# Kernel optimization log

Measured on AMD Instinct MI355X. Metric: run time of the kernel, lower is better.

Reference implementation:

```python
import jax, jax.numpy as jnp
import numpy as np

BATCH, SEQ, DIM, NH = 2, 4096, 1024, 16
HD = DIM // NH
BLOCK = 64


def setup_inputs() -> dict:
    key = jax.random.key(0)
    ks = jax.random.split(key, 8)
    x = jax.random.normal(ks[0], (BATCH, SEQ, DIM), dtype=jnp.float32)
    # standard RoPE tables: (seq, head_dim)
    inv_freq = 1.0 / (10000.0 ** (jnp.arange(0, HD, 2, dtype=jnp.float32) / HD))
    t = jnp.arange(SEQ, dtype=jnp.float32)
    freqs = jnp.outer(t, inv_freq)                      # (SEQ, HD//2)
    emb = jnp.concatenate([freqs, freqs], axis=-1)      # (SEQ, HD)
    cos, sin = jnp.cos(emb), jnp.sin(emb)
    s = 0.02
    wq = jax.random.normal(ks[1], (DIM, DIM), jnp.float32) * s
    wk = jax.random.normal(ks[2], (DIM, DIM), jnp.float32) * s
    wv = jax.random.normal(ks[3], (DIM, DIM), jnp.float32) * s
    wo = jax.random.normal(ks[4], (DIM, DIM), jnp.float32) * s
    A_log = jax.random.normal(ks[5], (NH,), jnp.float32) * 0.1
    w_dt_w = jax.random.normal(ks[6], (DIM, NH), jnp.float32) * s
    w_dt_b = jnp.zeros((NH,), jnp.float32)
    return {"x": x, "cos": cos, "sin": sin, "wq": wq, "wk": wk, "wv": wv,
            "wo": wo, "A_log": A_log, "w_dt_w": w_dt_w, "w_dt_b": w_dt_b}


def segsum(a):
    """a: (..., T) -> (..., T, T) lower-triangular segment sums, -inf above diag."""
    T = a.shape[-1]
    cs = jnp.cumsum(a, axis=-1)
    seg = cs[..., :, None] - cs[..., None, :]
    mask = jnp.tril(jnp.ones((T, T), dtype=bool))
    return jnp.where(mask, seg, -jnp.inf)


def rotate_half(t):
    t1, t2 = jnp.split(t, 2, axis=-1)
    return jnp.concatenate([-t2, t1], axis=-1)


def ssd(X, A, B, C, block_len):
    """Mamba-2 SSD chunked scan.
    X: (b,l,h,p)  A: (b,l,h)  B,C: (b,l,h,n)
    """
    b, l, h, p = X.shape
    c = l // block_len
    Xc = X.reshape(b, c, block_len, h, p)
    Bc = B.reshape(b, c, block_len, h, -1)
    Cc = C.reshape(b, c, block_len, h, -1)
    Ac = jnp.transpose(A.reshape(b, c, block_len, h), (0, 3, 1, 2))  # (b,h,c,l)
    A_cumsum = jnp.cumsum(Ac, axis=-1)
    # intra-chunk (diagonal block) output
    L = jnp.exp(segsum(Ac))                                          # (b,h,c,l,l)
    Y_diag = jnp.einsum('bclhn,bcshn,bhcls,bcshp->bclhp', Cc, Bc, L, Xc)
    # per-chunk states
    decay_states = jnp.exp(A_cumsum[:, :, :, -1:] - A_cumsum)        # (b,h,c,l)
    states = jnp.einsum('bclhn,bhcl,bclhp->bchpn', Bc, decay_states, Xc)
    init = jnp.zeros_like(states[:, :1])
    states = jnp.concatenate([init, states], axis=1)                 # (b,c+1,h,p,n)
    # inter-chunk recurrence (done as a 1-SS matmul over chunk axis)
    A_last = jnp.pad(A_cumsum[:, :, :, -1], ((0, 0), (0, 0), (1, 0)))
    decay_chunk = jnp.exp(segsum(A_last))                            # (b,h,c+1,c+1)
    new_states = jnp.einsum('bhzc,bchpn->bzhpn', decay_chunk, states)
    states, final_state = new_states[:, :-1], new_states[:, -1]
    # state -> output contribution
    state_decay_out = jnp.exp(A_cumsum)
    Y_off = jnp.einsum('bclhn,bchpn,bhcl->bclhp', Cc, states, state_decay_out)
    Y = (Y_diag + Y_off).reshape(b, l, h, p)
    return Y, final_state


def reference(x, cos, sin, wq, wk, wv, wo, A_log, w_dt_w, w_dt_b):
    b, l, dim = x.shape
    h = A_log.shape[0]
    d = dim // h
    xq = (x @ wq).reshape(b, l, h, d)
    xk = (x @ wk).reshape(b, l, h, d)
    xv = (x @ wv).reshape(b, l, h, d)
    cb = cos[None, :, None, :]
    sb = sin[None, :, None, :]
    xq = xq * cb + rotate_half(xq) * sb
    xk = xk * cb + rotate_half(xk) * sb
    dt = jax.nn.softplus(x @ w_dt_w + w_dt_b)           # (b,l,h)
    A = -jnp.exp(A_log)[None, None, :] * dt             # (b,l,h)
    X = xv * dt[..., None]                              # (b,l,h,d)
    Y, state = ssd(X, A, xk, xq, BLOCK)
    # replicate torch's transpose(1,2).view(b, l, -1) exactly:
    y = jnp.transpose(Y, (0, 2, 1, 3)).reshape(b, l, h * d)
    return y @ wo, state
```

## Files before the change

kernel.cpp:

```cpp
#include <hip/hip_runtime.h>


typedef __bf16 bf16x8 __attribute__((ext_vector_type(8)));
typedef float f32x4 __attribute__((ext_vector_type(4)));
typedef unsigned int u32x4 __attribute__((ext_vector_type(4)));
typedef unsigned short u16x8 __attribute__((ext_vector_type(8)));
typedef unsigned short u16x4 __attribute__((ext_vector_type(4)));

__device__ __forceinline__ unsigned short f2bf(float f) {
  unsigned int u = __builtin_bit_cast(unsigned int, f);
  u += 0x7fffu + ((u >> 16) & 1u);
  return (unsigned short)(u >> 16);
}
__device__ __forceinline__ float bf2f(unsigned short s) {
  unsigned int u = ((unsigned int)s) << 16;
  return __builtin_bit_cast(float, u);
}

#define GLOAD16(gp, lp)                                                \
  __builtin_amdgcn_global_load_lds(                                    \
      (const __attribute__((address_space(1))) void*)(gp),             \
      (__attribute__((address_space(3))) void*)(lp), 16, 0, 0)

__global__ __launch_bounds__(256) void convert_bf16_kernel(
    const float* __restrict__ in, unsigned short* __restrict__ out, int n4,
    const float* __restrict__ wdt, unsigned short* __restrict__ wdt_bf) {
  const int bx = blockIdx.x;
  if (bx < 8192) {
    int g = bx * 256 + threadIdx.x;
    if (g < n4) {
      f32x4 v = *reinterpret_cast<const f32x4*>(in + (size_t)g * 4);
      u16x4 o;
      o.x = f2bf(v.x); o.y = f2bf(v.y); o.z = f2bf(v.z); o.w = f2bf(v.w);
      *reinterpret_cast<u16x4*>(out + (size_t)g * 4) = o;
    }
  } else {
    const int g = (bx - 8192) * 256 + threadIdx.x;
    const int n = g >> 10, k = g & 1023;
    wdt_bf[g] = f2bf(wdt[k * 16 + n]);
  }
}

__global__ __launch_bounds__(256) void transpose_w_kernel(
    const float* __restrict__ w0, const float* __restrict__ w1,
    const float* __restrict__ w2, const float* __restrict__ w3,
    unsigned short* __restrict__ wt) {
  __shared__ float tile[32][33];
  const int z = blockIdx.z;
  const float* w = (z == 0) ? w0 : (z == 1) ? w1 : (z == 2) ? w2 : w3;
  unsigned short* o = wt + (size_t)z * 1024 * 1024;
  const int bx = blockIdx.x, by = blockIdx.y;
  const int tx = threadIdx.x, ty = threadIdx.y;
#pragma unroll
  for (int i = 0; i < 4; ++i)
    tile[ty + i * 8][tx] = w[(size_t)(by * 32 + ty + i * 8) * 1024 + bx * 32 + tx];
  __syncthreads();
#pragma unroll
  for (int i = 0; i < 4; ++i)
    o[(size_t)(bx * 32 + ty + i * 8) * 1024 + by * 32 + tx] = f2bf(tile[tx][ty + i * 8]);
}

__global__ __launch_bounds__(256) void dt_gemm_kernel(
    const unsigned short* __restrict__ A,
    const unsigned short* __restrict__ Bt,
    const float* __restrict__ bdt, float* __restrict__ dt) {
  __shared__ unsigned short As[2 * 64 * 32];
  const int tid = threadIdx.x, lane = tid & 63, w = tid >> 6;
  const int m0 = blockIdx.x * 64;
  const unsigned short* ga =
      A + (size_t)(m0 + w * 16 + (lane >> 2)) * 1024 + (lane & 3) * 8;
  unsigned short* la = As + w * 512;
  const int lr = lane & 15, lk = (lane >> 4) * 8;
  const unsigned short* gb = Bt + (size_t)lr * 1024 + lk;
  f32x4 acc = {};
  for (int kt = 0; kt < 1024; kt += 64) {
    GLOAD16(ga + kt, la);
    GLOAD16(ga + kt + 32, la + 2048);
    bf16x8 bF0 = *reinterpret_cast<const bf16x8*>(gb + kt);
    bf16x8 bF1 = *reinterpret_cast<const bf16x8*>(gb + kt + 32);
    __syncthreads();
    bf16x8 aF0 = *reinterpret_cast<const bf16x8*>(&As[(w * 16 + lr) * 32 + lk]);
    bf16x8 aF1 = *reinterpret_cast<const bf16x8*>(&As[2048 + (w * 16 + lr) * 32 + lk]);
    acc = __builtin_amdgcn_mfma_f32_16x16x32_bf16(aF0, bF0, acc, 0, 0, 0);
    acc = __builtin_amdgcn_mfma_f32_16x16x32_bf16(aF1, bF1, acc, 0, 0, 0);
    __syncthreads();
  }
  const int h = lr;
  const float bv = bdt[h];
#pragma unroll
  for (int r = 0; r < 4; ++r) {
    const int row = m0 + w * 16 + (lane >> 4) * 4 + r;
    const float a = acc[r] + bv;
    const float sp = (a > 0.f) ? (a + log1pf(expf(-a))) : log1pf(expf(a));
    dt[(size_t)row * 16 + h] = sp;
  }
}

template <int EPI>
__global__ __launch_bounds__(256) void gemm128_kernel(
    const unsigned short* __restrict__ A, const unsigned short* __restrict__ Bt,
    void* __restrict__ out0, unsigned short* __restrict__ out1,
    unsigned short* __restrict__ out2, const float* __restrict__ cosb,
    const float* __restrict__ sinb, const float* __restrict__ dtb) {
  __shared__ unsigned short As[128 * 64];
  __shared__ unsigned short Bs[128 * 64];
  const int tid = threadIdx.x, lane = tid & 63, w = tid >> 6;
  const int m0 = blockIdx.y * 128, n0 = blockIdx.x * 128;
  const int rw = lane >> 3;
  const int cu = ((lane & 7) ^ rw) * 8;
  const unsigned short* ga = A + (size_t)(m0 + w * 8 + rw) * 1024 + cu;
  const unsigned short* gb = Bt + (size_t)(n0 + w * 8 + rw) * 1024 + cu;
  unsigned short* la = As + (w * 8) * 64;
  unsigned short* lb = Bs + (w * 8) * 64;
  const int lr = lane & 15, lku = lane >> 4;
  const int wr = w >> 1, wc = w & 1;
  const int xr = lr & 7;
  f32x4 acc[4][4] = {};
  for (int kt = 0; kt < 1024; kt += 64) {
#pragma unroll
    for (int g = 0; g < 4; ++g) {
      GLOAD16(ga + kt + (size_t)(g * 32) * 1024, la + g * 32 * 64);
      GLOAD16(gb + kt + (size_t)(g * 32) * 1024, lb + g * 32 * 64);
    }
    __syncthreads();
#pragma unroll
    for (int kk = 0; kk < 2; ++kk) {
      const int un = (kk * 4 + lku) ^ xr;
      bf16x8 aF[4], bF[4];
#pragma unroll
      for (int i = 0; i < 4; ++i) {
        aF[i] = *reinterpret_cast<const bf16x8*>(&As[(wr * 64 + i * 16 + lr) * 64 + un * 8]);
        bF[i] = *reinterpret_cast<const bf16x8*>(&Bs[(wc * 64 + i * 16 + lr) * 64 + un * 8]);
      }
#pragma unroll
      for (int i = 0; i < 4; ++i)
#pragma unroll
        for (int j = 0; j < 4; ++j)
          acc[i][j] = __builtin_amdgcn_mfma_f32_16x16x32_bf16(aF[i], bF[j], acc[i][j], 0, 0, 0);
    }
    __syncthreads();
  }
  const int r0 = m0 + wr * 64 + ((lane >> 4) << 2);
  if constexpr (EPI == 0) {
    float* O = (float*)out0;
    const int c0 = n0 + wc * 64 + lr;
#pragma unroll
    for (int i = 0; i < 4; ++i)
#pragma unroll
      for (int j = 0; j < 4; ++j)
#pragma unroll
        for (int r = 0; r < 4; ++r)
          O[(size_t)(r0 + i * 16 + r) * 1024 + c0 + j * 16] = acc[i][j][r];
  } else {
    const int col = n0 + wc * 64;
    if (col < 2048) {
      unsigned short* O = (col < 1024) ? (unsigned short*)out0 : out1;
      const int cbase = col & 1023;
#pragma unroll
      for (int i = 0; i < 4; ++i)
#pragma unroll
        for (int jj = 0; jj < 2; ++jj) {
          const int d1 = jj * 16 + lr;
#pragma unroll
          for (int r = 0; r < 4; ++r) {
            const int row = r0 + i * 16 + r;
            const int l = row & 4095;
            const float cv = cosb[(size_t)l * 64 + d1];
            const float sv = sinb[(size_t)l * 64 + d1];
            const float v1 = acc[i][jj][r], v2 = acc[i][jj + 2][r];
            O[(size_t)row * 1024 + cbase + jj * 16 + lr] = f2bf(v1 * cv - v2 * sv);
            O[(size_t)row * 1024 + cbase + jj * 16 + lr + 32] = f2bf(v2 * cv + v1 * sv);
          }
        }
    } else {
      unsigned short* O = out2;
      const int cbase = col - 2048;
      const int h = cbase >> 6;
#pragma unroll
      for (int i = 0; i < 4; ++i)
#pragma unroll
        for (int r = 0; r < 4; ++r) {
          const int row = r0 + i * 16 + r;
          const float dtv = dtb[(size_t)row * 16 + h];
#pragma unroll
          for (int j = 0; j < 4; ++j)
            O[(size_t)row * 1024 + cbase + j * 16 + lr] = f2bf(acc[i][j][r] * dtv);
        }
    }
  }
}

__global__ __launch_bounds__(256) void ssd_states_kernel(
    const unsigned short* __restrict__ Kb, const unsigned short* __restrict__ Xb,
    const float* __restrict__ dtb, const float* __restrict__ A_log,
    unsigned short* __restrict__ chunk_states, float* __restrict__ chunk_dec) {
  __shared__ unsigned short T1[64 * 72], T2[64 * 72];
  __shared__ unsigned short BtL[64 * 72], XdL[64 * 72];
  __shared__ float csL[64], decL[64];
  const int c = blockIdx.x, h = blockIdx.y, b = blockIdx.z;
  const int tid = threadIdx.x, lane = tid & 63, w = tid >> 6;
  const size_t gbase = ((size_t)(b * 4096 + c * 64)) * 1024 + h * 64;
  {
    const int s = tid >> 2, e0 = (tid & 3) * 16;
    const unsigned short* gk = Kb + gbase + (size_t)s * 1024 + e0;
    const unsigned short* gx = Xb + gbase + (size_t)s * 1024 + e0;
    *(u32x4*)&T1[s * 72 + e0] = *(const u32x4*)gk;
    *(u32x4*)&T1[s * 72 + e0 + 8] = *(const u32x4*)(gk + 8);
    *(u32x4*)&T2[s * 72 + e0] = *(const u32x4*)gx;
    *(u32x4*)&T2[s * 72 + e0 + 8] = *(const u32x4*)(gx + 8);
  }
  if (w == 0) {
    float a = -expf(A_log[h]) * dtb[((size_t)(b * 4096 + c * 64 + lane)) * 16 + h];
    float v = a;
#pragma unroll
    for (int d = 1; d < 64; d <<= 1) {
      float o = __shfl_up(v, d, 64);
      if (lane >= d) v += o;
    }
    const float tot = __shfl(v, 63, 64);
    csL[lane] = v;
    decL[lane] = expf(tot - v);
    if (lane == 0) chunk_dec[((size_t)(b * 16 + h)) * 64 + c] = expf(tot);
  }
  __syncthreads();
#pragma unroll
  for (int q = 0; q < 2; ++q) {
    const int p = lane;
    const int s0 = (q * 4 + w) * 8;
    u16x8 vb, vx;
#pragma unroll
    for (int j = 0; j < 8; ++j) {
      vb[j] = T1[(s0 + j) * 72 + p];
      vx[j] = f2bf(bf2f(T2[(s0 + j) * 72 + p]) * decL[s0 + j]);
    }
    *(u16x8*)&BtL[p * 72 + s0] = vb;
    *(u16x8*)&XdL[p * 72 + s0] = vx;
  }
  __syncthreads();
  const int lr = lane & 15, lk = (lane >> 4) * 8;
  f32x4 acc[4] = {};
#pragma unroll
  for (int kt = 0; kt < 64; kt += 32) {
    bf16x8 aF = *reinterpret_cast<const bf16x8*>(&XdL[(w * 16 + lr) * 72 + kt + lk]);
#pragma unroll
    for (int j = 0; j < 4; ++j) {
      bf16x8 bF = *reinterpret_cast<const bf16x8*>(&BtL[(j * 16 + lr) * 72 + kt + lk]);
      acc[j] = __builtin_amdgcn_mfma_f32_16x16x32_bf16(aF, bF, acc[j], 0, 0, 0);
    }
  }
  const size_t stb = ((size_t)((b * 64 + c) * 16 + h)) * 4096;
#pragma unroll
  for (int j = 0; j < 4; ++j)
#pragma unroll
    for (int r = 0; r < 4; ++r)
      chunk_states[stb + (size_t)(w * 16 + (lane >> 4) * 4 + r) * 64 + j * 16 + lr] =
          f2bf(acc[j][r]);
}

__global__ __launch_bounds__(256) void scan_kernel(
    const unsigned short* __restrict__ chunk_states, const float* __restrict__ chunk_dec,
    unsigned short* __restrict__ inc_bf, float* __restrict__ state_out) {
  __shared__ float decs[64];
  const int g = blockIdx.x * 256 + threadIdx.x;
  const int n = g & 63, p = (g >> 6) & 63, h = (g >> 12) & 15, b = g >> 16;
  if (threadIdx.x < 64)
    decs[threadIdx.x] = chunk_dec[(size_t)((blockIdx.x * 256) >> 12 & 15) * 64 +
                                  (size_t)(blockIdx.x >> 8) * 1024 + threadIdx.x];
  __syncthreads();
  const size_t pn = (size_t)p * 64 + n;
  const size_t stride = (size_t)16 * 4096;
  const size_t base0 = ((size_t)(b * 64) * 16 + h) * 4096 + pn;
  float inc = 0.f;
  float cur = bf2f(chunk_states[base0]);
  for (int c = 0; c < 64; ++c) {
    const size_t idx = base0 + (size_t)c * stride;
    inc_bf[idx] = f2bf(inc);
    float nxt = (c < 63) ? bf2f(chunk_states[idx + stride]) : 0.f;
    inc = decs[c] * inc + cur;
    cur = nxt;
  }
  state_out[((size_t)(b * 16 + h) * 64 + p) * 64 + n] = inc;
}

__global__ __launch_bounds__(256) void ssd_y_kernel(
    const unsigned short* __restrict__ Qb, const unsigned short* __restrict__ Kb,
    const unsigned short* __restrict__ Xb, const unsigned short* __restrict__ Sg,
    const float* __restrict__ dtb, const float* __restrict__ A_log,
    unsigned short* __restrict__ y_bf) {
  __shared__ unsigned short Cb[64 * 72], Bb[64 * 72], Sb[64 * 72];
  __shared__ unsigned short Xt[64 * 72], TG[64 * 72];
  __shared__ float csL[64], sdeL[64];
  const int c = blockIdx.x, h = blockIdx.y, b = blockIdx.z;
  const int tid = threadIdx.x, lane = tid & 63, w = tid >> 6;
  const size_t gbase = ((size_t)(b * 4096 + c * 64)) * 1024 + h * 64;
  const size_t sbase = ((size_t)((b * 64 + c) * 16 + h)) * 4096;
  {
    const int s = tid >> 2, e0 = (tid & 3) * 16;
    const unsigned short* gq = Qb + gbase + (size_t)s * 1024 + e0;
    const unsigned short* gk = Kb + gbase + (size_t)s * 1024 + e0;
    const unsigned short* gx = Xb + gbase + (size_t)s * 1024 + e0;
    const unsigned short* gs = Sg + sbase + (size_t)s * 64 + e0;
    *(u32x4*)&Cb[s * 72 + e0] = *(const u32x4*)gq;
    *(u32x4*)&Cb[s * 72 + e0 + 8] = *(const u32x4*)(gq + 8);
    *(u32x4*)&Bb[s * 72 + e0] = *(const u32x4*)gk;
    *(u32x4*)&Bb[s * 72 + e0 + 8] = *(const u32x4*)(gk + 8);
    *(u32x4*)&TG[s * 72 + e0] = *(const u32x4*)gx;
    *(u32x4*)&TG[s * 72 + e0 + 8] = *(const u32x4*)(gx + 8);
    *(u32x4*)&Sb[s * 72 + e0] = *(const u32x4*)gs;
    *(u32x4*)&Sb[s * 72 + e0 + 8] = *(const u32x4*)(gs + 8);
  }
  if (w == 0) {
    float a = -expf(A_log[h]) * dtb[((size_t)(b * 4096 + c * 64 + lane)) * 16 + h];
    float v = a;
#pragma unroll
    for (int d = 1; d < 64; d <<= 1) {
      float o = __shfl_up(v, d, 64);
      if (lane >= d) v += o;
    }
    csL[lane] = v;
    sdeL[lane] = expf(v);
  }
  __syncthreads();
  const int lr = lane & 15, lk = (lane >> 4) * 8;
  f32x4 g[4] = {};
#pragma unroll
  for (int kt = 0; kt < 64; kt += 32) {
    bf16x8 aF = *reinterpret_cast<const bf16x8*>(&Cb[(w * 16 + lr) * 72 + kt + lk]);
#pragma unroll
    for (int j = 0; j < 4; ++j) {
      bf16x8 bF = *reinterpret_cast<const bf16x8*>(&Bb[(j * 16 + lr) * 72 + kt + lk]);
      g[j] = __builtin_amdgcn_mfma_f32_16x16x32_bf16(aF, bF, g[j], 0, 0, 0);
    }
  }
#pragma unroll
  for (int q = 0; q < 2; ++q) {
    const int p = lane;
    const int s0 = (q * 4 + w) * 8;
    u16x8 vx;
#pragma unroll
    for (int j = 0; j < 8; ++j) vx[j] = TG[(s0 + j) * 72 + p];
    *(u16x8*)&Xt[p * 72 + s0] = vx;
  }
  __syncthreads();
#pragma unroll
  for (int j = 0; j < 4; ++j)
#pragma unroll
    for (int r = 0; r < 4; ++r) {
      const int l = w * 16 + (lane >> 4) * 4 + r;
      const int s = j * 16 + lr;
      const float gm = (l >= s) ? g[j][r] * expf(csL[l] - csL[s]) : 0.f;
      TG[l * 72 + s] = f2bf(gm);
    }
  {
    const int rl = tid >> 2, e0 = (tid & 3) * 16;
    const float sde = sdeL[rl];
#pragma unroll
    for (int half = 0; half < 2; ++half) {
      u16x8 v = *(u16x8*)&Cb[rl * 72 + e0 + half * 8];
#pragma unroll
      for (int j = 0; j < 8; ++j) v[j] = f2bf(bf2f(v[j]) * sde);
      *(u16x8*)&Cb[rl * 72 + e0 + half * 8] = v;
    }
  }
  __syncthreads();
  f32x4 acc[4] = {};
#pragma unroll
  for (int kt = 0; kt < 64; kt += 32) {
    bf16x8 aG = *reinterpret_cast<const bf16x8*>(&TG[(w * 16 + lr) * 72 + kt + lk]);
    bf16x8 aC = *reinterpret_cast<const bf16x8*>(&Cb[(w * 16 + lr) * 72 + kt + lk]);
#pragma unroll
    for (int j = 0; j < 4; ++j) {
      bf16x8 bX = *reinterpret_cast<const bf16x8*>(&Xt[(j * 16 + lr) * 72 + kt + lk]);
      bf16x8 bS = *reinterpret_cast<const bf16x8*>(&Sb[(j * 16 + lr) * 72 + kt + lk]);
      acc[j] = __builtin_amdgcn_mfma_f32_16x16x32_bf16(aG, bX, acc[j], 0, 0, 0);
      acc[j] = __builtin_amdgcn_mfma_f32_16x16x32_bf16(aC, bS, acc[j], 0, 0, 0);
    }
  }
  const size_t orow = (size_t)b * 4096 + h * 256 + c * 4 + w;
#pragma unroll
  for (int j = 0; j < 4; ++j)
#pragma unroll
    for (int r = 0; r < 4; ++r) {
      const int li = (lane >> 4) * 4 + r;
      y_bf[orow * 1024 + li * 64 + j * 16 + lr] = f2bf(acc[j][r]);
    }
}

extern "C" void kernel_launch(void* const* d_in, const int* in_sizes, int n_in,
                              void* d_out, int out_size, void* d_ws, size_t ws_size,
                              hipStream_t stream) {
  (void)in_sizes; (void)n_in; (void)out_size; (void)ws_size;
  const float* x = (const float*)d_in[0];
  const float* cosb = (const float*)d_in[1];
  const float* sinb = (const float*)d_in[2];
  const float* wq = (const float*)d_in[3];
  const float* wk = (const float*)d_in[4];
  const float* wv = (const float*)d_in[5];
  const float* wo = (const float*)d_in[6];
  const float* A_log = (const float*)d_in[7];
  const float* wdt = (const float*)d_in[8];
  const float* bdt = (const float*)d_in[9];

  float* out_y = (float*)d_out;
  float* out_state = out_y + 8388608;

  const size_t MBB = 1048576;
  char* ws = (char*)d_ws;
  unsigned short* x_bf = (unsigned short*)(ws);
  unsigned short* w_t = (unsigned short*)(ws + 16 * MBB);
  unsigned short* q_bf = (unsigned short*)(ws + 24 * MBB);
  unsigned short* k_bf = (unsigned short*)(ws + 40 * MBB);
  unsigned short* xv_bf = (unsigned short*)(ws + 56 * MBB);
  float* dtb = (float*)(ws + 72 * MBB);
  unsigned short* wdt_bf = (unsigned short*)(ws + 73 * MBB);
  unsigned short* chunk_states = (unsigned short*)(ws + 74 * MBB);
  float* chunk_dec = (float*)(ws + 90 * MBB);
  unsigned short* inc_bf = (unsigned short*)(ws + 91 * MBB);

  convert_bf16_kernel<<<8256, 256, 0, stream>>>(x, x_bf, 2097152, wdt, wdt_bf);
  transpose_w_kernel<<<dim3(32, 32, 4), dim3(32, 8), 0, stream>>>(wq, wk, wv, wo, w_t);
  dt_gemm_kernel<<<128, 256, 0, stream>>>(x_bf, wdt_bf, bdt, dtb);

  gemm128_kernel<3><<<dim3(24, 64), 256, 0, stream>>>(
      x_bf, w_t, q_bf, k_bf, xv_bf, cosb, sinb, dtb);

  ssd_states_kernel<<<dim3(64, 16, 2), 256, 0, stream>>>(k_bf, xv_bf, dtb, A_log,
                                                         chunk_states, chunk_dec);
  scan_kernel<<<512, 256, 0, stream>>>(chunk_states, chunk_dec, inc_bf, out_state);
  ssd_y_kernel<<<dim3(64, 16, 2), 256, 0, stream>>>(q_bf, k_bf, xv_bf, inc_bf, dtb, A_log,
                                                    x_bf );

  gemm128_kernel<0><<<dim3(8, 64), 256, 0, stream>>>(
      x_bf , w_t + 3 * MBB, out_y, nullptr, nullptr, nullptr, nullptr, nullptr);
}
```

Before: 162.4 us.

## Merge conversion and weight-transpose kernels, deepen scan prefetch, tidy swizzle index

Combines the x/w_dt bf16 conversion and the four weight transposes into one prep kernel launch, so one launch and the gap between the two kernels go away. The scan kernel now prefetches chunk states two iterations ahead instead of one, to hide more load latency in its serial loop. The GEMM swizzle offset is precomputed in element units, which is cosmetic. The merged kernel uses a block-index branch with shared memory used only in the transpose path.

```diff
diff --git a/kernel.cpp b/kernel.cpp
--- a/kernel.cpp
+++ b/kernel.cpp
@@ -22,42 +22,40 @@
       (const __attribute__((address_space(1))) void*)(gp),             \
       (__attribute__((address_space(3))) void*)(lp), 16, 0, 0)
 
-__global__ __launch_bounds__(256) void convert_bf16_kernel(
-    const float* __restrict__ in, unsigned short* __restrict__ out, int n4,
-    const float* __restrict__ wdt, unsigned short* __restrict__ wdt_bf) {
-  const int bx = blockIdx.x;
-  if (bx < 8192) {
-    int g = bx * 256 + threadIdx.x;
-    if (g < n4) {
-      f32x4 v = *reinterpret_cast<const f32x4*>(in + (size_t)g * 4);
-      u16x4 o;
-      o.x = f2bf(v.x); o.y = f2bf(v.y); o.z = f2bf(v.z); o.w = f2bf(v.w);
-      *reinterpret_cast<u16x4*>(out + (size_t)g * 4) = o;
-    }
-  } else {
-    const int g = (bx - 8192) * 256 + threadIdx.x;
-    const int n = g >> 10, k = g & 1023;
-    wdt_bf[g] = f2bf(wdt[k * 16 + n]);
-  }
-}
-
-__global__ __launch_bounds__(256) void transpose_w_kernel(
+__global__ __launch_bounds__(256) void prep_kernel(
+    const float* __restrict__ x, unsigned short* __restrict__ x_bf,
+    const float* __restrict__ wdt, unsigned short* __restrict__ wdt_bf,
     const float* __restrict__ w0, const float* __restrict__ w1,
     const float* __restrict__ w2, const float* __restrict__ w3,
     unsigned short* __restrict__ wt) {
-  __shared__ float tile[32][33];
-  const int z = blockIdx.z;
-  const float* w = (z == 0) ? w0 : (z == 1) ? w1 : (z == 2) ? w2 : w3;
-  unsigned short* o = wt + (size_t)z * 1024 * 1024;
-  const int bx = blockIdx.x, by = blockIdx.y;
-  const int tx = threadIdx.x, ty = threadIdx.y;
-#pragma unroll
-  for (int i = 0; i < 4; ++i)
-    tile[ty + i * 8][tx] = w[(size_t)(by * 32 + ty + i * 8) * 1024 + bx * 32 + tx];
-  __syncthreads();
-#pragma unroll
-  for (int i = 0; i < 4; ++i)
-    o[(size_t)(bx * 32 + ty + i * 8) * 1024 + by * 32 + tx] = f2bf(tile[tx][ty + i * 8]);
+  const int bx = blockIdx.x;
+  const int tid = threadIdx.x;
+  if (bx < 8192) {
+    const int g = bx * 256 + tid;
+    f32x4 v = *reinterpret_cast<const f32x4*>(x + (size_t)g * 4);
+    u16x4 o;
+    o.x = f2bf(v.x); o.y = f2bf(v.y); o.z = f2bf(v.z); o.w = f2bf(v.w);
+    *reinterpret_cast<u16x4*>(x_bf + (size_t)g * 4) = o;
+  } else if (bx < 8256) {
+    const int g = (bx - 8192) * 256 + tid;
+    const int n = g >> 10, k = g & 1023;
+    wdt_bf[g] = f2bf(wdt[k * 16 + n]);
+  } else {
+    __shared__ float tile[32][33];
+    const int t = bx - 8256;
+    const int z = t >> 10, by = (t >> 5) & 31, bxx = t & 31;
+    const float* w = (z == 0) ? w0 : (z == 1) ? w1 : (z == 2) ? w2 : w3;
+    unsigned short* o = wt + (size_t)z * 1024 * 1024;
+    const int tx = tid & 31, ty = tid >> 5;
+#pragma unroll
+    for (int i = 0; i < 4; ++i)
+      tile[ty + i * 8][tx] = w[(size_t)(by * 32 + ty + i * 8) * 1024 + bxx * 32 + tx];
+    __syncthreads();
+#pragma unroll
+    for (int i = 0; i < 4; ++i)
+      o[(size_t)(bxx * 32 + ty + i * 8) * 1024 + by * 32 + tx] =
+          f2bf(tile[tx][ty + i * 8]);
+  }
 }
 
 __global__ __launch_bounds__(256) void dt_gemm_kernel(
@@ -125,12 +123,12 @@
     __syncthreads();
 #pragma unroll
     for (int kk = 0; kk < 2; ++kk) {
-      const int un = (kk * 4 + lku) ^ xr;
+      const int un = (((kk * 4 + lku) ^ xr) * 8);
       bf16x8 aF[4], bF[4];
 #pragma unroll
       for (int i = 0; i < 4; ++i) {
-        aF[i] = *reinterpret_cast<const bf16x8*>(&As[(wr * 64 + i * 16 + lr) * 64 + un * 8]);
-        bF[i] = *reinterpret_cast<const bf16x8*>(&Bs[(wc * 64 + i * 16 + lr) * 64 + un * 8]);
+        aF[i] = *reinterpret_cast<const bf16x8*>(&As[(wr * 64 + i * 16 + lr) * 64 + un]);
+        bF[i] = *reinterpret_cast<const bf16x8*>(&Bs[(wc * 64 + i * 16 + lr) * 64 + un]);
       }
 #pragma unroll
       for (int i = 0; i < 4; ++i)
@@ -271,13 +269,15 @@
   const size_t stride = (size_t)16 * 4096;
   const size_t base0 = ((size_t)(b * 64) * 16 + h) * 4096 + pn;
   float inc = 0.f;
-  float cur = bf2f(chunk_states[base0]);
+  float cur0 = bf2f(chunk_states[base0]);
+  float cur1 = bf2f(chunk_states[base0 + stride]);
   for (int c = 0; c < 64; ++c) {
     const size_t idx = base0 + (size_t)c * stride;
     inc_bf[idx] = f2bf(inc);
-    float nxt = (c < 63) ? bf2f(chunk_states[idx + stride]) : 0.f;
-    inc = decs[c] * inc + cur;
-    cur = nxt;
+    float nxt = (c < 62) ? bf2f(chunk_states[idx + 2 * stride]) : 0.f;
+    inc = decs[c] * inc + cur0;
+    cur0 = cur1;
+    cur1 = nxt;
   }
   state_out[((size_t)(b * 16 + h) * 64 + p) * 64 + n] = inc;
 }
@@ -417,8 +417,7 @@
   float* chunk_dec = (float*)(ws + 90 * MBB);
   unsigned short* inc_bf = (unsigned short*)(ws + 91 * MBB);
 
-  convert_bf16_kernel<<<8256, 256, 0, stream>>>(x, x_bf, 2097152, wdt, wdt_bf);
-  transpose_w_kernel<<<dim3(32, 32, 4), dim3(32, 8), 0, stream>>>(wq, wk, wv, wo, w_t);
+  prep_kernel<<<12352, 256, 0, stream>>>(x, x_bf, wdt, wdt_bf, wq, wk, wv, wo, w_t);
   dt_gemm_kernel<<<128, 256, 0, stream>>>(x_bf, wdt_bf, bdt, dtb);
 
   gemm128_kernel<3><<<dim3(24, 64), 256, 0, stream>>>(
```

After: 164.5 us. Within noise of the previous version (+1.3%).
